# Kernel optimization log

Hardware: AMD Instinct MI355X
Metric: run time of the kernel (lower is better)

Reference implementation:

```python
import jax, jax.numpy as jnp
import numpy as np

H = 1024          # n_hidden
FGB = 1.0         # forget_gate_bias added to forget-gate preactivation


def lstm_layer(x, h0, c0, Wih, Whh, b):
    """Standard LSTM over time-major x:(U,B,H). Gate order i,f,g,o (PyTorch)."""
    def step(carry, xt):
        h, c = carry
        gates = xt @ Wih.T + h @ Whh.T + b            # (B,4H)
        i, f, g, o = jnp.split(gates, 4, axis=-1)
        i = jax.nn.sigmoid(i)
        f = jax.nn.sigmoid(f + FGB)
        g = jnp.tanh(g)
        o = jax.nn.sigmoid(o)
        c = f * c + i * g
        h = o * jnp.tanh(c)
        return (h, c), h
    (hT, cT), hs = jax.lax.scan(step, (h0, c0), x)
    return hs, hT, cT


def setup_inputs() -> dict:
    key = jax.random.key(0)
    ks = jax.random.split(key, 8)
    B, U, V = 64, 512, 1024
    s = 1.0 / np.sqrt(H)
    inp = {
        "y": jax.random.randint(ks[0], (B, U), 0, V - 1, dtype=jnp.int64)
             if jax.config.jax_enable_x64 else
             jax.random.randint(ks[0], (B, U), 0, V - 1, dtype=jnp.int32),
        "E": jax.random.normal(ks[1], (V - 1, H), jnp.float32) * s,
        "Wih0": jax.random.normal(ks[2], (4 * H, H), jnp.float32) * s,
        "Whh0": jax.random.normal(ks[3], (4 * H, H), jnp.float32) * s,
        "b0": jax.random.normal(ks[4], (4 * H,), jnp.float32) * s,
        "Wih1": jax.random.normal(ks[5], (4 * H, H), jnp.float32) * s,
        "Whh1": jax.random.normal(ks[6], (4 * H, H), jnp.float32) * s,
        "b1": jax.random.normal(ks[7], (4 * H,), jnp.float32) * s,
    }
    return inp


def reference(y, E, Wih0, Whh0, b0, Wih1, Whh1, b1):
    # Prediction.forward with y given, state=None (zero initial states)
    x = E[y]                          # (B,U,H) embedding lookup
    x = jnp.transpose(x, (1, 0, 2))   # (U,B,H) time-major
    B = x.shape[1]
    z = jnp.zeros((B, H), x.dtype)
    hs0, h0f, c0f = lstm_layer(x, z, z, Wih0, Whh0, b0)
    hs1, h1f, c1f = lstm_layer(hs0, z, z, Wih1, Whh1, b1)
    g = jnp.transpose(hs1, (1, 0, 2))  # (B,U,H)
    h = jnp.stack([h0f, h1f])          # (L,B,H)
    c = jnp.stack([c0f, c1f])          # (L,B,H)
    return g, (h, c)
```

## Files before the change

kernel.cpp:

```cpp
#include <hip/hip_runtime.h>
#include <hip/hip_bf16.h>

typedef unsigned short u16;
typedef unsigned long long ull;
typedef __attribute__((ext_vector_type(8))) short bf16x8;
typedef __attribute__((ext_vector_type(4))) float f32x4;
typedef __attribute__((ext_vector_type(2))) float f32x2;

#define HID 1024
#define BATCH 64
#define SEQ 512
#define MTOK 32768

#define WB_WIH0 0
#define WB_WHH0 4194304
#define WB_WIH1 8388608
#define WB_WHH1 12582912
#define WS_X_OFF   33554432ull
#define WS_XP_OFF  100663296ull
#define WS_NEEDED  369098752ull
#define RING0_B 0ull
#define RING1_B 524288ull
#define XP1_B   1048576ull
#define FLAGS_B 3145728ull

#define OUT_H_OFF 33554432
#define OUT_C_OFF 33685504

__device__ __forceinline__ u16 f2bf(float f) {
    union { float f; unsigned u; } x; x.f = f;
    unsigned r = (x.u + 0x7FFFu + ((x.u >> 16) & 1u)) >> 16;
    return (u16)r;
}
__device__ __forceinline__ float bf2f(u16 v) {
    union { unsigned u; float f; } x; x.u = ((unsigned)v) << 16;
    return x.f;
}
__device__ __forceinline__ float fexp2(float x) { return __builtin_amdgcn_exp2f(x); }
__device__ __forceinline__ float frcp(float x) { return __builtin_amdgcn_rcpf(x); }
__device__ __forceinline__ float sigm(float x) {
    return frcp(1.f + fexp2(x * -1.4426950408889634f));
}
__device__ __forceinline__ float tanh_f(float x) {
    return 1.f - 2.f * frcp(fexp2(x * 2.8853900817779268f) + 1.f);
}
__device__ __forceinline__ float xhalf(unsigned r, int u) {
    return bf2f(u ? (u16)(r >> 16) : (u16)(r & 0xffffu));
}
__device__ __forceinline__ void ldsload16(const u16* g, u16* l) {
    __builtin_amdgcn_global_load_lds(
        (__attribute__((address_space(1))) void*)(unsigned long long)(const char*)g,
        (__attribute__((address_space(3))) void*)l, 16, 0, 0);
}
__device__ __forceinline__ ull ld8(const ull* p) {
    return __hip_atomic_load(p, __ATOMIC_RELAXED, __HIP_MEMORY_SCOPE_AGENT);
}
__device__ __forceinline__ unsigned ld4(const unsigned* p) {
    return __hip_atomic_load(p, __ATOMIC_RELAXED, __HIP_MEMORY_SCOPE_AGENT);
}
__device__ __forceinline__ void st8(ull* p, ull v) {
    __hip_atomic_store(p, v, __ATOMIC_RELAXED, __HIP_MEMORY_SCOPE_AGENT);
}
__device__ __forceinline__ void st4(unsigned* p, unsigned v) {
    __hip_atomic_store(p, v, __ATOMIC_RELAXED, __HIP_MEMORY_SCOPE_AGENT);
}

__launch_bounds__(256)
__global__ void prep_weights(const float* __restrict__ a, const float* __restrict__ b,
                             const float* __restrict__ c, const float* __restrict__ d,
                             u16* __restrict__ dst) {
    const int gtid = blockIdx.x * 256 + threadIdx.x;
#pragma unroll
    for (int k = 0; k < 16; k++) {
        const float* s = (k < 4) ? a : (k < 8) ? b : (k < 12) ? c : d;
        const int off = ((k & 3) * 262144 + gtid) * 4;
        float4 v = *(const float4*)(s + off);
        ushort4 o;
        o.x = f2bf(v.x); o.y = f2bf(v.y); o.z = f2bf(v.z); o.w = f2bf(v.w);
        *(ushort4*)(dst + (size_t)(k >> 2) * 4194304 + off) = o;
    }
}

__launch_bounds__(256)
__global__ void gather_x(const int* __restrict__ y, const float* __restrict__ E,
                         u16* __restrict__ X) {
    const int m = blockIdx.x;
    const int t = m >> 6, b = m & 63;
    const int idx = y[b * SEQ + t];
    const float4 v = *(const float4*)(E + (size_t)idx * HID + threadIdx.x * 4);
    ushort4 o;
    o.x = f2bf(v.x); o.y = f2bf(v.y); o.z = f2bf(v.z); o.w = f2bf(v.w);
    *(ushort4*)(X + (size_t)m * HID + threadIdx.x * 4) = o;
}

__launch_bounds__(256, 3)
__global__ void gemm_bt(const u16* __restrict__ A, const u16* __restrict__ Bm,
                        const float* __restrict__ bias, u16* __restrict__ C,
                        int M, int N, int K) {
    __shared__ u16 As[128 * 64];
    __shared__ u16 Bs[128 * 64];
    const int tid = threadIdx.x;
    const int ln = tid & 63;
    const int l15 = ln & 15, q = ln >> 4;
    const int w = tid >> 6;
    const int wm = (w & 1) * 64, wn = (w >> 1) * 64;
    const int m0 = blockIdx.y * 128, n0 = blockIdx.x * 128;

    f32x4 acc[4][4];
#pragma unroll
    for (int i = 0; i < 4; i++)
#pragma unroll
        for (int j = 0; j < 4; j++) acc[i][j] = 0.f;

    const int srow = tid >> 3;
    const int spk = tid & 7;
    const u16* gA = A + (size_t)m0 * K;
    const u16* gB = Bm + (size_t)n0 * K;
    const int wbase = (tid & 0xC0) * 8;

    const int kIters = K >> 6;
    for (int kt = 0; kt < kIters; kt++) {
        const int k0 = kt << 6;
        __syncthreads();
#pragma unroll
        for (int i = 0; i < 4; i++) {
            const int row = i * 32 + srow;
            const int kb = spk ^ (row & 7);
            ldsload16(gA + (size_t)row * K + k0 + kb * 8, &As[i * 2048 + wbase]);
            ldsload16(gB + (size_t)row * K + k0 + kb * 8, &Bs[i * 2048 + wbase]);
        }
        __syncthreads();
#pragma unroll
        for (int s = 0; s < 2; s++) {
            const int xk = ((s * 4 + q) ^ (l15 & 7)) * 8;
            bf16x8 af[4], bfr[4];
#pragma unroll
            for (int mi = 0; mi < 4; mi++)
                af[mi] = *(const bf16x8*)&As[(wm + mi * 16 + l15) * 64 + xk];
#pragma unroll
            for (int nj = 0; nj < 4; nj++)
                bfr[nj] = *(const bf16x8*)&Bs[(wn + nj * 16 + l15) * 64 + xk];
#pragma unroll
            for (int mi = 0; mi < 4; mi++)
#pragma unroll
                for (int nj = 0; nj < 4; nj++)
                    acc[mi][nj] = __builtin_amdgcn_mfma_f32_16x16x32_bf16(
                        af[mi], bfr[nj], acc[mi][nj], 0, 0, 0);
        }
    }
#pragma unroll
    for (int nj = 0; nj < 4; nj++) {
        const int n = n0 + wn + nj * 16 + l15;
        const float bv = bias[n];
#pragma unroll
        for (int mi = 0; mi < 4; mi++) {
            const size_t m = (size_t)(m0 + wm + mi * 16 + q * 4);
            u16* cp = C + m * N + n;
            f32x4 v = acc[mi][nj];
            cp[0]           = f2bf(v.x + bv);
            cp[(size_t)N]   = f2bf(v.y + bv);
            cp[(size_t)2*N] = f2bf(v.z + bv);
            cp[(size_t)3*N] = f2bf(v.w + bv);
        }
    }
}

__global__ void init_flags(unsigned* f) { if (threadIdx.x < 192) f[threadIdx.x] = 0; }


__device__ __forceinline__ void load_wf(const u16* W, int j0, int w, int l15, int q,
                                        bf16x8 wf[4][8]) {
    const u16* wbase = W + (size_t)(j0 + l15) * HID + w * 256 + q * 8;
#pragma unroll
    for (int nt = 0; nt < 4; nt++)
#pragma unroll
        for (int ki = 0; ki < 8; ki++)
            wf[nt][ki] = *(const bf16x8*)(wbase + (size_t)nt * 1048576 + ki * 32);
}

__device__ __forceinline__ void mm_ring(const u16* slab, const bf16x8 wf[4][8],
                                        int w, int l15, int q, float (*P)[64][68]) {
    union BU { ull v[2]; bf16x8 f; };
    BU st[4][8];
    const u16* arow = slab + (size_t)l15 * HID + w * 256 + q * 8;
#pragma unroll
    for (int ki = 0; ki < 8; ki++)
#pragma unroll
        for (int mt = 0; mt < 4; mt++) {
            const ull* p = (const ull*)(arow + mt * 16384 + ki * 32);
            st[mt][ki].v[0] = ld8(p);
            st[mt][ki].v[1] = ld8(p + 1);
        }
    f32x4 acc[4][4];
#pragma unroll
    for (int mt = 0; mt < 4; mt++)
#pragma unroll
        for (int nt = 0; nt < 4; nt++) acc[mt][nt] = 0.f;
#pragma unroll
    for (int ki = 0; ki < 8; ki++)
#pragma unroll
        for (int mt = 0; mt < 4; mt++)
#pragma unroll
            for (int nt = 0; nt < 4; nt++)
                acc[mt][nt] = __builtin_amdgcn_mfma_f32_16x16x32_bf16(
                    st[mt][ki].f, wf[nt][ki], acc[mt][nt], 0, 0, 0);
#pragma unroll
    for (int mt = 0; mt < 4; mt++)
#pragma unroll
        for (int nt = 0; nt < 4; nt++)
            *(f32x4*)&P[w][nt * 16 + l15][mt * 16 + q * 4] = acc[mt][nt];
}

__device__ __forceinline__ void waitflags(const unsigned* F0, const unsigned* Fp,
                                          const unsigned* Fr, int n0, int np, int nr,
                                          int w, int ln, int* abortf) {
    const unsigned* A = (w == 0) ? F0 : (w == 1) ? Fp : Fr;
    const int need = (w == 0) ? n0 : (w == 1) ? np : nr;
    if (w < 3 && need > 0 && *abortf == 0) {
        int it = 0;
        while ((int)ld4(&A[ln]) < need) {
            if (++it > 20000000) { *abortf = 1; break; }
        }
    }
    __syncthreads();
}

__launch_bounds__(256, 1)
__global__ void pipeline(const u16* __restrict__ wb, const u16* __restrict__ Xp,
                         const float* __restrict__ b1, float* __restrict__ out,
                         u16* __restrict__ ring0, u16* __restrict__ ring1,
                         u16* __restrict__ xp1, unsigned* __restrict__ flags) {
    __shared__ float P[4][64][68];
    __shared__ int abortf;
    const int tid = threadIdx.x;
    if (tid == 0) abortf = 0;
    const int w = tid >> 6, ln = tid & 63;
    const int l15 = ln & 15, q = ln >> 4;
    const int bid = blockIdx.x;
    const int role = bid >> 6;
    const int j0 = (bid & 63) * 16;
    unsigned* F0 = flags;
    unsigned* Fp = flags + 64;
    unsigned* Fr = flags + 128;
    __syncthreads();

    bf16x8 wf[4][8];

    if (role == 0) {
        load_wf(wb + WB_WHH0, j0, w, l15, q, wf);
        const int up = tid & 7, bp = tid >> 3;
        float cst[2][2] = {{0.f, 0.f}, {0.f, 0.f}};
        for (int r = 0; r < 512; ++r) {
            unsigned xraw[4][2];
            const u16* xr = Xp + (size_t)(r * 64 + bp * 2) * 4096 + j0 + up * 2;
#pragma unroll
            for (int bb = 0; bb < 2; bb++)
#pragma unroll
                for (int gg = 0; gg < 4; gg++)
                    xraw[gg][bb] = *(const unsigned*)(xr + (size_t)bb * 4096 + gg * 1024);
            waitflags(F0, Fp, Fr, r, r - 2, 0, w, ln, &abortf);
            if (r > 0)
                mm_ring(ring0 + (size_t)((r - 1) & 3) * 65536, wf, w, l15, q, P);
            __syncthreads();
            f32x2 pre[4][2];
#pragma unroll
            for (int gg = 0; gg < 4; gg++)
#pragma unroll
                for (int u = 0; u < 2; u++) {
                    if (r > 0) {
                        const int col = gg * 16 + up * 2 + u;
                        f32x2 s = *(const f32x2*)&P[0][col][bp * 2];
                        s += *(const f32x2*)&P[1][col][bp * 2];
                        s += *(const f32x2*)&P[2][col][bp * 2];
                        s += *(const f32x2*)&P[3][col][bp * 2];
                        pre[gg][u] = s;
                    } else pre[gg][u] = 0.f;
                }
            u16* hout = ring0 + (size_t)(r & 3) * 65536;
#pragma unroll
            for (int bb = 0; bb < 2; bb++) {
                const int b = bp * 2 + bb;
                float hn[2], cn[2];
#pragma unroll
                for (int u = 0; u < 2; u++) {
                    const float pi = pre[0][u][bb] + xhalf(xraw[0][bb], u);
                    const float pf = pre[1][u][bb] + xhalf(xraw[1][bb], u) + 1.0f;
                    const float pg = pre[2][u][bb] + xhalf(xraw[2][bb], u);
                    const float po = pre[3][u][bb] + xhalf(xraw[3][bb], u);
                    const float cnew = sigm(pf) * cst[bb][u] + sigm(pi) * tanh_f(pg);
                    cst[bb][u] = cnew;
                    hn[u] = sigm(po) * tanh_f(cnew);
                    cn[u] = cnew;
                }
                const unsigned hw = (unsigned)f2bf(hn[0]) | ((unsigned)f2bf(hn[1]) << 16);
                st4((unsigned*)(hout + (size_t)b * HID + j0 + up * 2), hw);
                if (r == 511) {
                    f32x2 h2 = {hn[0], hn[1]}, c2 = {cn[0], cn[1]};
                    *(f32x2*)&out[OUT_H_OFF + (size_t)b * HID + j0 + up * 2] = h2;
                    *(f32x2*)&out[OUT_C_OFF + (size_t)b * HID + j0 + up * 2] = c2;
                }
            }
            __syncthreads();
            if (tid == 0) st4(&F0[bid], (unsigned)(r + 1));
        }
    } else if (role == 1) {
        load_wf(wb + WB_WIH1, j0, w, l15, q, wf);
        const int ucol = tid & 15, bq = tid >> 4;
        float bv[4];
#pragma unroll
        for (int gg = 0; gg < 4; gg++) bv[gg] = b1[gg * 1024 + j0 + ucol];
        for (int r = 1; r <= 512; ++r) {
            waitflags(F0, Fp, Fr, r, 0, r - 2, w, ln, &abortf);
            mm_ring(ring0 + (size_t)((r - 1) & 3) * 65536, wf, w, l15, q, P);
            __syncthreads();
            u16* xo = xp1 + (size_t)((r - 1) & 3) * 262144;
#pragma unroll
            for (int gg = 0; gg < 4; gg++) {
                const int col = gg * 16 + ucol;
                f32x4 s = *(const f32x4*)&P[0][col][bq * 4];
                s += *(const f32x4*)&P[1][col][bq * 4];
                s += *(const f32x4*)&P[2][col][bq * 4];
                s += *(const f32x4*)&P[3][col][bq * 4];
                s += bv[gg];
                const ull hw = (ull)f2bf(s.x) | ((ull)f2bf(s.y) << 16)
                             | ((ull)f2bf(s.z) << 32) | ((ull)f2bf(s.w) << 48);
                st8((ull*)(xo + (size_t)(gg * 1024 + j0 + ucol) * 64 + bq * 4), hw);
            }
            __syncthreads();
            if (tid == 0) st4(&Fp[bid & 63], (unsigned)(r + 1));
        }
    } else {
        load_wf(wb + WB_WHH1, j0, w, l15, q, wf);
        const int up = tid & 7, bp = tid >> 3;
        float cst[2][2] = {{0.f, 0.f}, {0.f, 0.f}};
        for (int r = 2; r <= 513; ++r) {
            const int t = r - 2;
            waitflags(F0, Fp, Fr, 0, r, (r >= 3) ? r : 0, w, ln, &abortf);
            unsigned xr2[4][2];
            const u16* xb = xp1 + (size_t)(t & 3) * 262144;
#pragma unroll
            for (int gg = 0; gg < 4; gg++)
#pragma unroll
                for (int u = 0; u < 2; u++)
                    xr2[gg][u] = ld4((const unsigned*)(xb +
                        (size_t)(gg * 1024 + j0 + up * 2 + u) * 64 + bp * 2));
            if (r > 2)
                mm_ring(ring1 + (size_t)((r - 3) & 3) * 65536, wf, w, l15, q, P);
            __syncthreads();
            f32x2 pre[4][2];
#pragma unroll
            for (int gg = 0; gg < 4; gg++)
#pragma unroll
                for (int u = 0; u < 2; u++) {
                    if (r > 2) {
                        const int col = gg * 16 + up * 2 + u;
                        f32x2 s = *(const f32x2*)&P[0][col][bp * 2];
                        s += *(const f32x2*)&P[1][col][bp * 2];
                        s += *(const f32x2*)&P[2][col][bp * 2];
                        s += *(const f32x2*)&P[3][col][bp * 2];
                        pre[gg][u] = s;
                    } else pre[gg][u] = 0.f;
                }
            u16* hout = ring1 + (size_t)((r - 2) & 3) * 65536;
#pragma unroll
            for (int bb = 0; bb < 2; bb++) {
                const int b = bp * 2 + bb;
                float hn[2], cn[2];
#pragma unroll
                for (int u = 0; u < 2; u++) {
                    const float pi = pre[0][u][bb] + xhalf(xr2[0][u], bb);
                    const float pf = pre[1][u][bb] + xhalf(xr2[1][u], bb) + 1.0f;
                    const float pg = pre[2][u][bb] + xhalf(xr2[2][u], bb);
                    const float po = pre[3][u][bb] + xhalf(xr2[3][u], bb);
                    const float cnew = sigm(pf) * cst[bb][u] + sigm(pi) * tanh_f(pg);
                    cst[bb][u] = cnew;
                    hn[u] = sigm(po) * tanh_f(cnew);
                    cn[u] = cnew;
                }
                const unsigned hw = (unsigned)f2bf(hn[0]) | ((unsigned)f2bf(hn[1]) << 16);
                st4((unsigned*)(hout + (size_t)b * HID + j0 + up * 2), hw);
                f32x2 g2 = {hn[0], hn[1]};
                *(f32x2*)&out[(size_t)b * 524288 + (size_t)t * 1024 + j0 + up * 2] = g2;
                if (r == 513) {
                    f32x2 h2 = {hn[0], hn[1]}, c2 = {cn[0], cn[1]};
                    *(f32x2*)&out[OUT_H_OFF + 65536 + (size_t)b * HID + j0 + up * 2] = h2;
                    *(f32x2*)&out[OUT_C_OFF + 65536 + (size_t)b * HID + j0 + up * 2] = c2;
                }
            }
            __syncthreads();
            if (tid == 0) st4(&Fr[bid & 63], (unsigned)(r + 1));
        }
    }
}

__global__ void diag(float* o, float v) { o[0] = v; }

extern "C" void kernel_launch(void* const* d_in, const int* in_sizes, int n_in,
                              void* d_out, int out_size, void* d_ws, size_t ws_size,
                              hipStream_t stream) {
    const int*   y    = (const int*)  d_in[0];
    const float* Emb  = (const float*)d_in[1];
    const float* Wih0 = (const float*)d_in[2];
    const float* Whh0 = (const float*)d_in[3];
    const float* b0   = (const float*)d_in[4];
    const float* Wih1 = (const float*)d_in[5];
    const float* Whh1 = (const float*)d_in[6];
    const float* b1   = (const float*)d_in[7];
    float* out = (float*)d_out;
    char* wsb = (char*)d_ws;

    if (ws_size < WS_NEEDED) {
        diag<<<1, 1, 0, stream>>>(out, (float)(ws_size >> 20));
        return;
    }

    u16* wb   = (u16*)wsb;
    u16* X    = (u16*)(wsb + WS_X_OFF);
    u16* Xp   = (u16*)(wsb + WS_XP_OFF);
    u16* ring0 = (u16*)(wsb + RING0_B);
    u16* ring1 = (u16*)(wsb + RING1_B);
    u16* xp1   = (u16*)(wsb + XP1_B);
    unsigned* flags = (unsigned*)(wsb + FLAGS_B);

    prep_weights<<<1024, 256, 0, stream>>>(Wih0, Whh0, Wih1, Whh1, wb);
    gather_x<<<MTOK, 256, 0, stream>>>(y, Emb, X);
    gemm_bt<<<dim3(32, 256), 256, 0, stream>>>(X, wb + WB_WIH0, b0, Xp, MTOK, 4096, HID);
    init_flags<<<1, 256, 0, stream>>>(flags);
    pipeline<<<192, 256, 0, stream>>>(wb, Xp, b1, out, ring0, ring1, xp1, flags);
}
```

Baseline: 6.788 ms.

## Store input-projection outputs in per-block contiguous layout for coalesced 8-byte loads

The GEMM epilogue now writes the precomputed layer-0 input projection in a layout blocked by hidden-unit block and thread, so each recurrent thread fetches its four gate values with contiguous 8-byte loads instead of eight scattered 4-byte loads. The layer-1 projection role writes xp1 in the same layout, so the layer-1 recurrence can also use 8-byte reads. This is meant to cut latency on the serial critical path of the recurrent steps. The spin-wait now sleeps briefly between polls and uses a lower timeout count, which reduces memory polling traffic but may add wake-up latency. The GEMM epilogue's scattered 2-byte stores may make that stage slower.

```diff
diff --git a/kernel.cpp b/kernel.cpp
--- a/kernel.cpp
+++ b/kernel.cpp
@@ -27,6 +27,7 @@
 #define OUT_H_OFF 33554432
 #define OUT_C_OFF 33685504
 
+
 __device__ __forceinline__ u16 f2bf(float f) {
     union { float f; unsigned u; } x; x.f = f;
     unsigned r = (x.u + 0x7FFFu + ((x.u >> 16) & 1u)) >> 16;
@@ -44,8 +45,8 @@
 __device__ __forceinline__ float tanh_f(float x) {
     return 1.f - 2.f * frcp(fexp2(x * 2.8853900817779268f) + 1.f);
 }
-__device__ __forceinline__ float xhalf(unsigned r, int u) {
-    return bf2f(u ? (u16)(r >> 16) : (u16)(r & 0xffffu));
+__device__ __forceinline__ float xpick(ull q, int bb, int u) {
+    return bf2f((u16)(q >> ((bb * 2 + u) << 4)));
 }
 __device__ __forceinline__ void ldsload16(const u16* g, u16* l) {
     __builtin_amdgcn_global_load_lds(
@@ -152,15 +153,22 @@
     for (int nj = 0; nj < 4; nj++) {
         const int n = n0 + wn + nj * 16 + l15;
         const float bv = bias[n];
+        const int g = n >> 10, c = n & 1023;
+        const int jblk = c >> 4, up = (c & 15) >> 1, u = c & 1;
 #pragma unroll
         for (int mi = 0; mi < 4; mi++) {
-            const size_t m = (size_t)(m0 + wm + mi * 16 + q * 4);
-            u16* cp = C + m * N + n;
+            const int mb = m0 + wm + mi * 16 + q * 4;
             f32x4 v = acc[mi][nj];
-            cp[0]           = f2bf(v.x + bv);
-            cp[(size_t)N]   = f2bf(v.y + bv);
-            cp[(size_t)2*N] = f2bf(v.z + bv);
-            cp[(size_t)3*N] = f2bf(v.w + bv);
+            float vals[4] = {v.x, v.y, v.z, v.w};
+#pragma unroll
+            for (int k = 0; k < 4; k++) {
+                const int m = mb + k;
+                const int r = m >> 6, b = m & 63;
+                const int bp = b >> 1, bb = b & 1;
+                const int t = bp * 8 + up;
+                C[(size_t)r * 262144 + jblk * 4096 + t * 16 + g * 4 + bb * 2 + u]
+                    = f2bf(vals[k] + bv);
+            }
         }
     }
 }
@@ -219,7 +227,8 @@
     if (w < 3 && need > 0 && *abortf == 0) {
         int it = 0;
         while ((int)ld4(&A[ln]) < need) {
-            if (++it > 20000000) { *abortf = 1; break; }
+            __builtin_amdgcn_s_sleep(1);
+            if (++it > 2000000) { *abortf = 1; break; }
         }
     }
     __syncthreads();
@@ -238,7 +247,8 @@
     const int l15 = ln & 15, q = ln >> 4;
     const int bid = blockIdx.x;
     const int role = bid >> 6;
-    const int j0 = (bid & 63) * 16;
+    const int jblk = bid & 63;
+    const int j0 = jblk * 16;
     unsigned* F0 = flags;
     unsigned* Fp = flags + 64;
     unsigned* Fr = flags + 128;
@@ -251,13 +261,10 @@
         const int up = tid & 7, bp = tid >> 3;
         float cst[2][2] = {{0.f, 0.f}, {0.f, 0.f}};
         for (int r = 0; r < 512; ++r) {
-            unsigned xraw[4][2];
-            const u16* xr = Xp + (size_t)(r * 64 + bp * 2) * 4096 + j0 + up * 2;
-#pragma unroll
-            for (int bb = 0; bb < 2; bb++)
-#pragma unroll
-                for (int gg = 0; gg < 4; gg++)
-                    xraw[gg][bb] = *(const unsigned*)(xr + (size_t)bb * 4096 + gg * 1024);
+            ull xq[4];
+            const ull* xp8 = (const ull*)(Xp + (size_t)r * 262144 + jblk * 4096 + tid * 16);
+#pragma unroll
+            for (int gg = 0; gg < 4; gg++) xq[gg] = xp8[gg];
             waitflags(F0, Fp, Fr, r, r - 2, 0, w, ln, &abortf);
             if (r > 0)
                 mm_ring(ring0 + (size_t)((r - 1) & 3) * 65536, wf, w, l15, q, P);
@@ -283,10 +290,10 @@
                 float hn[2], cn[2];
 #pragma unroll
                 for (int u = 0; u < 2; u++) {
-                    const float pi = pre[0][u][bb] + xhalf(xraw[0][bb], u);
-                    const float pf = pre[1][u][bb] + xhalf(xraw[1][bb], u) + 1.0f;
-                    const float pg = pre[2][u][bb] + xhalf(xraw[2][bb], u);
-                    const float po = pre[3][u][bb] + xhalf(xraw[3][bb], u);
+                    const float pi = pre[0][u][bb] + xpick(xq[0], bb, u);
+                    const float pf = pre[1][u][bb] + xpick(xq[1], bb, u) + 1.0f;
+                    const float pg = pre[2][u][bb] + xpick(xq[2], bb, u);
+                    const float po = pre[3][u][bb] + xpick(xq[3], bb, u);
                     const float cnew = sigm(pf) * cst[bb][u] + sigm(pi) * tanh_f(pg);
                     cst[bb][u] = cnew;
                     hn[u] = sigm(po) * tanh_f(cnew);
@@ -305,29 +312,40 @@
         }
     } else if (role == 1) {
         load_wf(wb + WB_WIH1, j0, w, l15, q, wf);
-        const int ucol = tid & 15, bq = tid >> 4;
-        float bv[4];
-#pragma unroll
-        for (int gg = 0; gg < 4; gg++) bv[gg] = b1[gg * 1024 + j0 + ucol];
+        const int up = tid & 7, bp = tid >> 3;
+        float bv[4][2];
+#pragma unroll
+        for (int gg = 0; gg < 4; gg++)
+#pragma unroll
+            for (int u = 0; u < 2; u++)
+                bv[gg][u] = b1[gg * 1024 + j0 + up * 2 + u];
         for (int r = 1; r <= 512; ++r) {
             waitflags(F0, Fp, Fr, r, 0, r - 2, w, ln, &abortf);
             mm_ring(ring0 + (size_t)((r - 1) & 3) * 65536, wf, w, l15, q, P);
             __syncthreads();
-            u16* xo = xp1 + (size_t)((r - 1) & 3) * 262144;
+            ull* xo8 = (ull*)(xp1 + (size_t)((r - 1) & 3) * 262144 + jblk * 4096 + tid * 16);
+            ull ow[4];
 #pragma unroll
             for (int gg = 0; gg < 4; gg++) {
-                const int col = gg * 16 + ucol;
-                f32x4 s = *(const f32x4*)&P[0][col][bq * 4];
-                s += *(const f32x4*)&P[1][col][bq * 4];
-                s += *(const f32x4*)&P[2][col][bq * 4];
-                s += *(const f32x4*)&P[3][col][bq * 4];
-                s += bv[gg];
-                const ull hw = (ull)f2bf(s.x) | ((ull)f2bf(s.y) << 16)
-                             | ((ull)f2bf(s.z) << 32) | ((ull)f2bf(s.w) << 48);
-                st8((ull*)(xo + (size_t)(gg * 1024 + j0 + ucol) * 64 + bq * 4), hw);
+                ow[gg] = 0;
+#pragma unroll
+                for (int u = 0; u < 2; u++) {
+                    const int col = gg * 16 + up * 2 + u;
+                    f32x2 s = *(const f32x2*)&P[0][col][bp * 2];
+                    s += *(const f32x2*)&P[1][col][bp * 2];
+                    s += *(const f32x2*)&P[2][col][bp * 2];
+                    s += *(const f32x2*)&P[3][col][bp * 2];
+#pragma unroll
+                    for (int bb = 0; bb < 2; bb++) {
+                        const float val = s[bb] + bv[gg][u];
+                        ow[gg] |= (ull)f2bf(val) << ((bb * 2 + u) << 4);
+                    }
+                }
             }
-            __syncthreads();
-            if (tid == 0) st4(&Fp[bid & 63], (unsigned)(r + 1));
+#pragma unroll
+            for (int gg = 0; gg < 4; gg++) st8(xo8 + gg, ow[gg]);
+            __syncthreads();
+            if (tid == 0) st4(&Fp[jblk], (unsigned)(r + 1));
         }
     } else {
         load_wf(wb + WB_WHH1, j0, w, l15, q, wf);
@@ -336,14 +354,10 @@
         for (int r = 2; r <= 513; ++r) {
             const int t = r - 2;
             waitflags(F0, Fp, Fr, 0, r, (r >= 3) ? r : 0, w, ln, &abortf);
-            unsigned xr2[4][2];
-            const u16* xb = xp1 + (size_t)(t & 3) * 262144;
-#pragma unroll
-            for (int gg = 0; gg < 4; gg++)
-#pragma unroll
-                for (int u = 0; u < 2; u++)
-                    xr2[gg][u] = ld4((const unsigned*)(xb +
-                        (size_t)(gg * 1024 + j0 + up * 2 + u) * 64 + bp * 2));
+            ull xq[4];
+            const ull* xp8 = (const ull*)(xp1 + (size_t)(t & 3) * 262144 + jblk * 4096 + tid * 16);
+#pragma unroll
+            for (int gg = 0; gg < 4; gg++) xq[gg] = ld8(xp8 + gg);
             if (r > 2)
                 mm_ring(ring1 + (size_t)((r - 3) & 3) * 65536, wf, w, l15, q, P);
             __syncthreads();
@@ -368,10 +382,10 @@
                 float hn[2], cn[2];
 #pragma unroll
                 for (int u = 0; u < 2; u++) {
-                    const float pi = pre[0][u][bb] + xhalf(xr2[0][u], bb);
-                    const float pf = pre[1][u][bb] + xhalf(xr2[1][u], bb) + 1.0f;
-                    const float pg = pre[2][u][bb] + xhalf(xr2[2][u], bb);
-                    const float po = pre[3][u][bb] + xhalf(xr2[3][u], bb);
+                    const float pi = pre[0][u][bb] + xpick(xq[0], bb, u);
+                    const float pf = pre[1][u][bb] + xpick(xq[1], bb, u) + 1.0f;
+                    const float pg = pre[2][u][bb] + xpick(xq[2], bb, u);
+                    const float po = pre[3][u][bb] + xpick(xq[3], bb, u);
                     const float cnew = sigm(pf) * cst[bb][u] + sigm(pi) * tanh_f(pg);
                     cst[bb][u] = cnew;
                     hn[u] = sigm(po) * tanh_f(cnew);
@@ -388,7 +402,7 @@
                 }
             }
             __syncthreads();
-            if (tid == 0) st4(&Fr[bid & 63], (unsigned)(r + 1));
+            if (tid == 0) st4(&Fr[jblk], (unsigned)(r + 1));
         }
     }
 }
```

New measurement: 6.968 ms. 1.03x slower.
